# Optimization experiments

Measured on AMD Instinct MI355X. Metric: run time of the kernel, lower is better.

The kernel has to match this reference:

```python
import jax, jax.numpy as jnp
import numpy as np

B, H, W, C = 16, 64, 64, 768
NH, KD = 12, 64           # num_heads, key_dim; C == NH*KD
NUM_AXES = 2              # attn_axes = [[1],[2]] -> heads split into 2 groups
SCALE = float(np.sqrt(KD))


def setup_inputs() -> dict:
    key = jax.random.key(0)
    ks = jax.random.split(key, 8)
    s = 0.02  # init scale for kernels
    return {
        "queries": jax.random.normal(ks[0], (B, H, W, C), dtype=jnp.float32),
        "values": jax.random.normal(ks[1], (B, H, W, C), dtype=jnp.float32),
        "Wq": jax.random.normal(ks[2], (C, NH, KD), dtype=jnp.float32) * s,
        "bq": jnp.zeros((NH, KD), dtype=jnp.float32),
        "Wk": jax.random.normal(ks[3], (C, NH, KD), dtype=jnp.float32) * s,
        "bk": jnp.zeros((NH, KD), dtype=jnp.float32),
        "Wv": jax.random.normal(ks[4], (C, NH, KD), dtype=jnp.float32) * s,
        "bv": jnp.zeros((NH, KD), dtype=jnp.float32),
        "Wo": jax.random.normal(ks[5], (NH, KD, C), dtype=jnp.float32) * s,
        "bo": jnp.zeros((C,), dtype=jnp.float32),
    }


def _attend_axis_h(q, k, v):
    # attention along the H axis (axis 1); q,k,v: [B,H,W,n,d]
    s = jnp.einsum('bxwnd,bhwnd->bwnhx', k, q) / SCALE  # [B,W,n,Hq,Hk]
    s = jax.nn.softmax(s, axis=-1)
    return jnp.einsum('bwnhx,bxwnd->bhwnd', s, v)


def _attend_axis_w(q, k, v):
    # attention along the W axis (axis 2); q,k,v: [B,H,W,n,d]
    s = jnp.einsum('bhynd,bhwnd->bhnwy', k, q) / SCALE  # [B,H,n,Wq,Wk]
    s = jax.nn.softmax(s, axis=-1)
    return jnp.einsum('bhnwy,bhynd->bhwnd', s, v)


def reference(queries, values, Wq, bq, Wk, bk, Wv, bv, Wo, bo):
    # QKV projections: [B,H,W,C] -> [B,H,W,NH,KD]
    q = jnp.einsum('bhwc,cnd->bhwnd', queries, Wq) + bq
    k = jnp.einsum('bhwc,cnd->bhwnd', values, Wk) + bk
    v = jnp.einsum('bhwc,cnd->bhwnd', values, Wv) + bv
    g = NH // NUM_AXES  # heads per axis group
    o0 = _attend_axis_h(q[..., :g, :], k[..., :g, :], v[..., :g, :])
    o1 = _attend_axis_w(q[..., g:, :], k[..., g:, :], v[..., g:, :])
    out = jnp.concatenate([o0, o1], axis=-2)  # [B,H,W,NH,KD]
    return jnp.einsum('bhwnd,ndc->bhwc', out, Wo) + bo
```

## Files before the change

kernel.cpp:

```cpp
#include <hip/hip_runtime.h>

typedef unsigned short u16;
typedef __bf16 bf16x8 __attribute__((ext_vector_type(8)));
typedef float f32x4 __attribute__((ext_vector_type(4)));

union BF8 {
    bf16x8 v;
    __bf16 e[8];
    u16 h[8];
};

typedef __attribute__((address_space(1))) void gvoid;
typedef __attribute__((address_space(3))) void lvoid;

__device__ __forceinline__ u16 f2bf(float f) {
    __bf16 h = (__bf16)f;
    return __builtin_bit_cast(u16, h);
}

__device__ __forceinline__ void gld_lds16(const void* g, void* l) {
    __builtin_amdgcn_global_load_lds((gvoid*)g, (lvoid*)l, 16, 0, 0);
}

__device__ __forceinline__ f32x4 mfma16(bf16x8 a, bf16x8 b, f32x4 c) {
    return __builtin_amdgcn_mfma_f32_16x16x32_bf16(a, b, c, 0, 0, 0);
}

__global__ __launch_bounds__(256) void transpose_cvt(const float* __restrict__ src,
                                                     u16* __restrict__ dst) {
    __shared__ float t[64][65];
    const int c0 = blockIdx.x * 64, r0 = blockIdx.y * 64;
    const int tid = threadIdx.x;
#pragma unroll
    for (int i = 0; i < 16; ++i) {
        int e = tid + 256 * i;
        int rr = e >> 6, cc = e & 63;
        t[rr][cc] = src[(r0 + rr) * 768 + c0 + cc];
    }
    __syncthreads();
#pragma unroll
    for (int i = 0; i < 16; ++i) {
        int e = tid + 256 * i;
        int rr = e >> 6, cc = e & 63;
        dst[(c0 + rr) * 768 + r0 + cc] = f2bf(t[cc][rr]);
    }
}

template <bool A_F32, bool OUT_F32>
__global__ __launch_bounds__(256) void gemm_kernel(const void* __restrict__ Aptr,
                                                   const u16* __restrict__ Bt,
                                                   const float* __restrict__ bias,
                                                   void* __restrict__ Out) {
    constexpr int ASMEM = A_F32 ? 16384 : 8192;
    __shared__ __attribute__((aligned(16))) char smem[ASMEM + 8192];
    float* Asf = (float*)smem;
    u16* Asb = (u16*)smem;
    u16* Bs = (u16*)(smem + ASMEM);

    const int tid = threadIdx.x;
    const int wid = tid >> 6, lane = tid & 63;
    const int quad = lane >> 4, lm = lane & 15;
    const int mbase = (wid >> 1) * 64, nbase = (wid & 1) * 64;
    const long row0 = (long)blockIdx.x * 128;
    const int n0 = blockIdx.y * 128;

    const f32x4 zero = {0.f, 0.f, 0.f, 0.f};
    f32x4 acc[4][4];
#pragma unroll
    for (int mi = 0; mi < 4; ++mi)
#pragma unroll
        for (int ni = 0; ni < 4; ++ni) acc[mi][ni] = zero;

    for (int kt = 0; kt < 24; ++kt) {
        const int k0 = kt * 32;
        if constexpr (A_F32) {
            const float* A = (const float*)Aptr;
#pragma unroll
            for (int i = 0; i < 4; ++i) {
                int chunk = tid + 256 * i;
                int m = chunk >> 3, kc = chunk & 7;
                gld_lds16(A + (row0 + m) * 768 + k0 + kc * 4, Asf + chunk * 4);
            }
        } else {
            const u16* A = (const u16*)Aptr;
#pragma unroll
            for (int i = 0; i < 2; ++i) {
                int chunk = tid + 256 * i;
                int m = chunk >> 2, kc = chunk & 3;
                gld_lds16(A + (row0 + m) * 768 + k0 + kc * 8, Asb + chunk * 8);
            }
        }
#pragma unroll
        for (int i = 0; i < 2; ++i) {
            int chunk = tid + 256 * i;
            int n = chunk >> 2, kc = chunk & 3;
            gld_lds16(Bt + (long)(n0 + n) * 768 + k0 + kc * 8, Bs + chunk * 8);
        }
        __syncthreads();

        bf16x8 af[4], bfr[4];
#pragma unroll
        for (int mi = 0; mi < 4; ++mi) {
            int m = mbase + mi * 16 + lm;
            if constexpr (A_F32) {
                const float* p = Asf + m * 32 + quad * 8;
                f32x4 x0 = *(const f32x4*)p;
                f32x4 x1 = *(const f32x4*)(p + 4);
                BF8 u;
#pragma unroll
                for (int j = 0; j < 4; ++j) {
                    u.e[j] = (__bf16)x0[j];
                    u.e[4 + j] = (__bf16)x1[j];
                }
                af[mi] = u.v;
            } else {
                af[mi] = *(const bf16x8*)(Asb + m * 32 + quad * 8);
            }
        }
#pragma unroll
        for (int ni = 0; ni < 4; ++ni)
            bfr[ni] = *(const bf16x8*)(Bs + (nbase + ni * 16 + lm) * 32 + quad * 8);
#pragma unroll
        for (int mi = 0; mi < 4; ++mi)
#pragma unroll
            for (int ni = 0; ni < 4; ++ni)
                acc[mi][ni] = mfma16(af[mi], bfr[ni], acc[mi][ni]);
        __syncthreads();
    }

#pragma unroll
    for (int mi = 0; mi < 4; ++mi) {
        const long row = row0 + mbase + mi * 16 + quad * 4;
#pragma unroll
        for (int ni = 0; ni < 4; ++ni) {
            const int n = n0 + nbase + ni * 16 + lm;
            const float bv = bias[n];
#pragma unroll
            for (int r = 0; r < 4; ++r) {
                float v = acc[mi][ni][r] + bv;
                if constexpr (OUT_F32)
                    ((float*)Out)[(row + r) * 768 + n] = v;
                else
                    ((u16*)Out)[(row + r) * 768 + n] = f2bf(v);
            }
        }
    }
}

__global__ __launch_bounds__(256) void attn_kernel(const u16* __restrict__ q,
                                                   const u16* __restrict__ k,
                                                   const u16* __restrict__ v,
                                                   u16* __restrict__ o) {
    __shared__ __attribute__((aligned(16))) u16 Qs[64 * 64];
    __shared__ __attribute__((aligned(16))) u16 Ks[64 * 64];
    __shared__ __attribute__((aligned(16))) u16 Vs[64 * 64];

    const int cross = blockIdx.x;
    const int b = blockIdx.y;
    const int head = blockIdx.z;
    const bool axis0 = head < 6;
    const int tid = threadIdx.x;
    const int wid = tid >> 6, lane = tid & 63;
    const int quad = lane >> 4, lm = lane & 15;

    const long base = (long)b * 4096 + (axis0 ? cross : cross * 64);
    const int pstride = axis0 ? 64 : 1;
    const int coloff = head * 64;

#pragma unroll
    for (int i = 0; i < 2; ++i) {
        int chunk = tid + 256 * i;
        int p = chunk >> 3, c = chunk & 7;
        long g = (base + (long)p * pstride) * 768 + coloff + c * 8;
        gld_lds16(q + g, Qs + chunk * 8);
        gld_lds16(k + g, Ks + chunk * 8);
        gld_lds16(v + g, Vs + chunk * 8);
    }
    __syncthreads();

    const f32x4 zero = {0.f, 0.f, 0.f, 0.f};
    f32x4 s[4];
#pragma unroll
    for (int nt = 0; nt < 4; ++nt) s[nt] = zero;

    bf16x8 qf[2];
#pragma unroll
    for (int kt = 0; kt < 2; ++kt)
        qf[kt] = *(const bf16x8*)(Qs + (16 * wid + lm) * 64 + kt * 32 + quad * 8);
#pragma unroll
    for (int nt = 0; nt < 4; ++nt)
#pragma unroll
        for (int kt = 0; kt < 2; ++kt) {
            bf16x8 kf = *(const bf16x8*)(Ks + (nt * 16 + lm) * 64 + kt * 32 + quad * 8);
            s[nt] = mfma16(qf[kt], kf, s[nt]);
        }

    float invl[4];
#pragma unroll
    for (int nt = 0; nt < 4; ++nt) s[nt] = s[nt] * 0.125f;
#pragma unroll
    for (int r = 0; r < 4; ++r) {
        float m = fmaxf(fmaxf(s[0][r], s[1][r]), fmaxf(s[2][r], s[3][r]));
#pragma unroll
        for (int d = 1; d < 16; d <<= 1) m = fmaxf(m, __shfl_xor(m, d));
        float l = 0.f;
#pragma unroll
        for (int nt = 0; nt < 4; ++nt) {
            float p = exp2f((s[nt][r] - m) * 1.44269504f);
            s[nt][r] = p;
            l += p;
        }
#pragma unroll
        for (int d = 1; d < 16; d <<= 1) l += __shfl_xor(l, d);
        invl[r] = 1.f / l;
    }

#pragma unroll
    for (int nt = 0; nt < 4; ++nt)
#pragma unroll
        for (int r = 0; r < 4; ++r)
            Qs[(16 * wid + quad * 4 + r) * 64 + nt * 16 + lm] = f2bf(s[nt][r]);
    __syncthreads();

    f32x4 oacc[4];
#pragma unroll
    for (int nt = 0; nt < 4; ++nt) oacc[nt] = zero;
#pragma unroll
    for (int kt = 0; kt < 2; ++kt) {
        bf16x8 pf = *(const bf16x8*)(Qs + (16 * wid + lm) * 64 + kt * 32 + quad * 8);
#pragma unroll
        for (int nt = 0; nt < 4; ++nt) {
            BF8 vu;
#pragma unroll
            for (int j = 0; j < 8; ++j)
                vu.h[j] = Vs[(kt * 32 + quad * 8 + j) * 64 + nt * 16 + lm];
            oacc[nt] = mfma16(pf, vu.v, oacc[nt]);
        }
    }

#pragma unroll
    for (int nt = 0; nt < 4; ++nt)
#pragma unroll
        for (int r = 0; r < 4; ++r) {
            int p = 16 * wid + quad * 4 + r;
            long grow = base + (long)p * pstride;
            o[grow * 768 + coloff + nt * 16 + lm] = f2bf(oacc[nt][r] * invl[r]);
        }
}

extern "C" void kernel_launch(void* const* d_in, const int* in_sizes, int n_in,
                              void* d_out, int out_size, void* d_ws, size_t ws_size,
                              hipStream_t stream) {
    const float* queries = (const float*)d_in[0];
    const float* values = (const float*)d_in[1];
    const float* Wq = (const float*)d_in[2];
    const float* bq = (const float*)d_in[3];
    const float* Wk = (const float*)d_in[4];
    const float* bk = (const float*)d_in[5];
    const float* Wv = (const float*)d_in[6];
    const float* bv = (const float*)d_in[7];
    const float* Wo = (const float*)d_in[8];
    const float* bo = (const float*)d_in[9];

    const long MAT = 65536L * 768;
    const long WMAT = 768L * 768;
    u16* qws = (u16*)d_ws;
    u16* kws = qws + MAT;
    u16* vws = kws + MAT;
    u16* aws = vws + MAT;
    u16* wtq = aws + MAT;
    u16* wtk = wtq + WMAT;
    u16* wtv = wtk + WMAT;
    u16* wto = wtv + WMAT;

    dim3 tb(256);
    dim3 tg(12, 12);
    transpose_cvt<<<tg, tb, 0, stream>>>(Wq, wtq);
    transpose_cvt<<<tg, tb, 0, stream>>>(Wk, wtk);
    transpose_cvt<<<tg, tb, 0, stream>>>(Wv, wtv);
    transpose_cvt<<<tg, tb, 0, stream>>>(Wo, wto);

    dim3 gg(512, 6);
    gemm_kernel<true, false><<<gg, tb, 0, stream>>>(queries, wtq, bq, qws);
    gemm_kernel<true, false><<<gg, tb, 0, stream>>>(values, wtk, bk, kws);
    gemm_kernel<true, false><<<gg, tb, 0, stream>>>(values, wtv, bv, vws);

    attn_kernel<<<dim3(64, 16, 12), tb, 0, stream>>>(qws, kws, vws, aws);

    gemm_kernel<false, true><<<gg, tb, 0, stream>>>(aws, wto, bo, (float*)d_out);
}
```

Baseline: 1.163 ms.

## Swizzle LDS tiles, transpose V in shared memory, reorder GEMM grid

Result: faster. 1.140 ms (-2.0%).

```diff
diff --git a/kernel.cpp b/kernel.cpp
--- a/kernel.cpp
+++ b/kernel.cpp
@@ -61,8 +61,8 @@
     const int wid = tid >> 6, lane = tid & 63;
     const int quad = lane >> 4, lm = lane & 15;
     const int mbase = (wid >> 1) * 64, nbase = (wid & 1) * 64;
-    const long row0 = (long)blockIdx.x * 128;
-    const int n0 = blockIdx.y * 128;
+    const long row0 = (long)blockIdx.y * 128;
+    const int n0 = blockIdx.x * 128;
 
     const f32x4 zero = {0.f, 0.f, 0.f, 0.f};
     f32x4 acc[4][4];
@@ -78,7 +78,8 @@
 #pragma unroll
             for (int i = 0; i < 4; ++i) {
                 int chunk = tid + 256 * i;
-                int m = chunk >> 3, kc = chunk & 7;
+                int m = chunk >> 3, s = chunk & 7;
+                int kc = s ^ (m & 7);
                 gld_lds16(A + (row0 + m) * 768 + k0 + kc * 4, Asf + chunk * 4);
             }
         } else {
@@ -86,14 +87,16 @@
 #pragma unroll
             for (int i = 0; i < 2; ++i) {
                 int chunk = tid + 256 * i;
-                int m = chunk >> 2, kc = chunk & 3;
+                int m = chunk >> 2, s = chunk & 3;
+                int kc = s ^ ((m >> 1) & 3);
                 gld_lds16(A + (row0 + m) * 768 + k0 + kc * 8, Asb + chunk * 8);
             }
         }
 #pragma unroll
         for (int i = 0; i < 2; ++i) {
             int chunk = tid + 256 * i;
-            int n = chunk >> 2, kc = chunk & 3;
+            int n = chunk >> 2, s = chunk & 3;
+            int kc = s ^ ((n >> 1) & 3);
             gld_lds16(Bt + (long)(n0 + n) * 768 + k0 + kc * 8, Bs + chunk * 8);
         }
         __syncthreads();
@@ -103,9 +106,10 @@
         for (int mi = 0; mi < 4; ++mi) {
             int m = mbase + mi * 16 + lm;
             if constexpr (A_F32) {
-                const float* p = Asf + m * 32 + quad * 8;
-                f32x4 x0 = *(const f32x4*)p;
-                f32x4 x1 = *(const f32x4*)(p + 4);
+                int c0 = m * 8 + ((quad * 2) ^ (m & 7));
+                int c1 = m * 8 + ((quad * 2 + 1) ^ (m & 7));
+                f32x4 x0 = *(const f32x4*)(Asf + c0 * 4);
+                f32x4 x1 = *(const f32x4*)(Asf + c1 * 4);
                 BF8 u;
 #pragma unroll
                 for (int j = 0; j < 4; ++j) {
@@ -114,12 +118,16 @@
                 }
                 af[mi] = u.v;
             } else {
-                af[mi] = *(const bf16x8*)(Asb + m * 32 + quad * 8);
+                int c = m * 4 + (quad ^ ((m >> 1) & 3));
+                af[mi] = *(const bf16x8*)(Asb + c * 8);
             }
         }
 #pragma unroll
-        for (int ni = 0; ni < 4; ++ni)
-            bfr[ni] = *(const bf16x8*)(Bs + (nbase + ni * 16 + lm) * 32 + quad * 8);
+        for (int ni = 0; ni < 4; ++ni) {
+            int n = nbase + ni * 16 + lm;
+            int c = n * 4 + (quad ^ ((n >> 1) & 3));
+            bfr[ni] = *(const bf16x8*)(Bs + c * 8);
+        }
 #pragma unroll
         for (int mi = 0; mi < 4; ++mi)
 #pragma unroll
@@ -154,6 +162,7 @@
     __shared__ __attribute__((aligned(16))) u16 Qs[64 * 64];
     __shared__ __attribute__((aligned(16))) u16 Ks[64 * 64];
     __shared__ __attribute__((aligned(16))) u16 Vs[64 * 64];
+    __shared__ __attribute__((aligned(16))) u16 Vt[64 * 72];
 
     const int cross = blockIdx.x;
     const int b = blockIdx.y;
@@ -170,7 +179,8 @@
 #pragma unroll
     for (int i = 0; i < 2; ++i) {
         int chunk = tid + 256 * i;
-        int p = chunk >> 3, c = chunk & 7;
+        int p = chunk >> 3, s = chunk & 7;
+        int c = s ^ (p & 7);
         long g = (base + (long)p * pstride) * 768 + coloff + c * 8;
         gld_lds16(q + g, Qs + chunk * 8);
         gld_lds16(k + g, Ks + chunk * 8);
@@ -178,6 +188,17 @@
     }
     __syncthreads();
 
+#pragma unroll
+    for (int i = 0; i < 2; ++i) {
+        int chunk = tid + 256 * i;
+        int pos = chunk & 63, cc = chunk >> 6;
+        int slot = pos * 8 + (cc ^ (pos & 7));
+        BF8 vv;
+        vv.v = *(const bf16x8*)(Vs + slot * 8);
+#pragma unroll
+        for (int j = 0; j < 8; ++j) Vt[(cc * 8 + j) * 72 + pos] = vv.h[j];
+    }
+
     const f32x4 zero = {0.f, 0.f, 0.f, 0.f};
     f32x4 s[4];
 #pragma unroll
@@ -185,13 +206,18 @@
 
     bf16x8 qf[2];
 #pragma unroll
-    for (int kt = 0; kt < 2; ++kt)
-        qf[kt] = *(const bf16x8*)(Qs + (16 * wid + lm) * 64 + kt * 32 + quad * 8);
+    for (int kt = 0; kt < 2; ++kt) {
+        int row = 16 * wid + lm;
+        int slot = row * 8 + ((kt * 4 + quad) ^ (row & 7));
+        qf[kt] = *(const bf16x8*)(Qs + slot * 8);
+    }
 #pragma unroll
     for (int nt = 0; nt < 4; ++nt)
 #pragma unroll
         for (int kt = 0; kt < 2; ++kt) {
-            bf16x8 kf = *(const bf16x8*)(Ks + (nt * 16 + lm) * 64 + kt * 32 + quad * 8);
+            int row = nt * 16 + lm;
+            int slot = row * 8 + ((kt * 4 + quad) ^ (row & 7));
+            bf16x8 kf = *(const bf16x8*)(Ks + slot * 8);
             s[nt] = mfma16(qf[kt], kf, s[nt]);
         }
 
@@ -218,8 +244,11 @@
 #pragma unroll
     for (int nt = 0; nt < 4; ++nt)
 #pragma unroll
-        for (int r = 0; r < 4; ++r)
-            Qs[(16 * wid + quad * 4 + r) * 64 + nt * 16 + lm] = f2bf(s[nt][r]);
+        for (int r = 0; r < 4; ++r) {
+            int h = 16 * wid + quad * 4 + r;
+            int c = nt * 2 + (lm >> 3);
+            Qs[(h * 8 + (c ^ (h & 7))) * 8 + (lm & 7)] = f2bf(s[nt][r]);
+        }
     __syncthreads();
 
     f32x4 oacc[4];
@@ -227,14 +256,13 @@
     for (int nt = 0; nt < 4; ++nt) oacc[nt] = zero;
 #pragma unroll
     for (int kt = 0; kt < 2; ++kt) {
-        bf16x8 pf = *(const bf16x8*)(Qs + (16 * wid + lm) * 64 + kt * 32 + quad * 8);
+        int row = 16 * wid + lm;
+        int slot = row * 8 + ((kt * 4 + quad) ^ (row & 7));
+        bf16x8 pf = *(const bf16x8*)(Qs + slot * 8);
 #pragma unroll
         for (int nt = 0; nt < 4; ++nt) {
-            BF8 vu;
-#pragma unroll
-            for (int j = 0; j < 8; ++j)
-                vu.h[j] = Vs[(kt * 32 + quad * 8 + j) * 64 + nt * 16 + lm];
-            oacc[nt] = mfma16(pf, vu.v, oacc[nt]);
+            bf16x8 vf = *(const bf16x8*)(Vt + (nt * 16 + lm) * 72 + kt * 32 + quad * 8);
+            oacc[nt] = mfma16(pf, vf, oacc[nt]);
         }
     }
 
@@ -280,7 +308,7 @@
     transpose_cvt<<<tg, tb, 0, stream>>>(Wv, wtv);
     transpose_cvt<<<tg, tb, 0, stream>>>(Wo, wto);
 
-    dim3 gg(512, 6);
+    dim3 gg(6, 512);
     gemm_kernel<true, false><<<gg, tb, 0, stream>>>(queries, wtq, bq, qws);
     gemm_kernel<true, false><<<gg, tb, 0, stream>>>(values, wtk, bk, kws);
     gemm_kernel<true, false><<<gg, tb, 0, stream>>>(values, wtv, bv, vws);
```
